# Optimization experiments

Measured on AMD Instinct MI355X. Metric: run time of the kernel, lower is better.

The kernel has to match this reference:

```python
import jax, jax.numpy as jnp
import numpy as np

MV = 16          # multivector dimension (PGA G(3,0,1))
BLADE_LEN = 9    # number of equivariant basis maps
# inner-product mask: coordinates not containing e0 (scalar, e1,e2,e3, e12,e13,e23, e123)
IP_IDX = np.array([0, 2, 3, 4, 8, 9, 10, 14])


def equi_linear(w, blade, x):
    """EquiLinearLayer: einsum('j i b, b x y, ... i x -> ... j y').
    Precompute blade-contracted weight once (fusion the kernel would do)."""
    wb = jnp.einsum('jib,bxy->jixy', w, blade)          # [J, I, MV, MV]
    return jnp.einsum('jixy,...ix->...jy', wb, x)        # [..., J, MV]


def setup_inputs() -> dict:
    key = jax.random.key(0)
    ks = jax.random.split(key, 6)
    B, N, C = 2, 2048, 64       # batch, items, mv_channels
    D, H = 64, 8                # hidden_dim, n_heads
    x = jax.random.normal(ks[0], (B, N, C, MV), dtype=jnp.float32)
    blade = jax.random.normal(ks[1], (BLADE_LEN, MV, MV), dtype=jnp.float32)
    w_q = jax.random.uniform(ks[2], (D * H, C, BLADE_LEN), dtype=jnp.float32)
    w_k = jax.random.uniform(ks[3], (D, C, BLADE_LEN), dtype=jnp.float32)
    w_v = jax.random.uniform(ks[4], (D, C, BLADE_LEN), dtype=jnp.float32)
    w_o = jax.random.uniform(ks[5], (C, D * H, BLADE_LEN), dtype=jnp.float32)
    return {"x": x, "blade": blade, "w_q": w_q, "w_k": w_k, "w_v": w_v, "w_o": w_o}


def reference(x, blade, w_q, w_k, w_v, w_o):
    B, N, C, _ = x.shape
    D = w_k.shape[0]
    H = w_q.shape[0] // D

    q = equi_linear(w_q, blade, x)   # [B, N, D*H, MV]
    k = equi_linear(w_k, blade, x)   # [B, N, D, MV]
    v = equi_linear(w_v, blade, x)   # [B, N, D, MV]

    # '(hidden_dim n_heads)' split: hidden_dim outer, heads inner
    q = q.reshape(B, N, D, H, MV).transpose(0, 3, 1, 2, 4)   # [B, H, N, D, MV]

    # select inner-product coordinates and flatten channel x coord
    qm = q[..., IP_IDX].reshape(B, H, N, D * len(IP_IDX))    # [B, H, N, D*8]
    km = k[..., IP_IDX].reshape(B, N, D * len(IP_IDX))        # [B, N, D*8]
    vf = v.reshape(B, N, D * MV)                              # [B, N, D*16]

    scale = 1.0 / jnp.sqrt(jnp.asarray(qm.shape[-1], qm.dtype))
    scores = jnp.einsum('bhqe,bke->bhqk', qm, km) * scale     # [B, H, N, N]
    attn = jax.nn.softmax(scores, axis=-1)
    out = jnp.einsum('bhqk,bkf->bhqf', attn, vf)              # [B, H, N, D*16]

    # slice first hidden_dim*mv (a no-op here since v keeps all 16 coords)
    out = out[..., : D * MV].reshape(B, H, N, D, MV)
    # '(heads hidden_dim)': heads outer
    out = out.transpose(0, 2, 1, 3, 4).reshape(B, N, H * D, MV)

    return equi_linear(w_o, blade, out)                       # [B, N, out_channels, MV]
```

## Files before the change

kernel.cpp:

```cpp
#include <hip/hip_runtime.h>
#include <math.h>


typedef __bf16 bf16x8 __attribute__((ext_vector_type(8)));
typedef __bf16 bf16x4 __attribute__((ext_vector_type(4)));
typedef float floatx4 __attribute__((ext_vector_type(4)));
typedef float floatx16 __attribute__((ext_vector_type(16)));

__constant__ int c_ip[8] = {0, 2, 3, 4, 8, 9, 10, 14};

__global__ __launch_bounds__(256) void prep2(
    const float* __restrict__ x, const float* __restrict__ blade,
    const float* __restrict__ w_q, const float* __restrict__ w_k,
    const float* __restrict__ w_v, const float* __restrict__ w_o,
    __bf16* __restrict__ xh, __bf16* __restrict__ xl,
    __bf16* __restrict__ wbqkh, __bf16* __restrict__ wbqkl,
    __bf16* __restrict__ wbv, __bf16* __restrict__ wbo)
{
  __shared__ float sw[4608];
  __shared__ float sbl[144];
  const int blk = blockIdx.x;
  const int tid = threadIdx.x;

  if (blk < 4608) {
    int n = blk;
    const float* wrow;
    int y;
    if (n < 4096) {
      int e = n & 7, d = (n >> 3) & 63, h = n >> 9;
      wrow = w_q + (size_t)(d * 8 + h) * 576;
      y = c_ip[e];
    } else {
      int n2 = n - 4096;
      int e = n2 & 7, d = n2 >> 3;
      wrow = w_k + (size_t)d * 576;
      y = c_ip[e];
    }
    for (int t = tid; t < 576; t += 256) sw[t] = wrow[t];
    if (tid < 144) sbl[tid] = blade[(tid >> 4) * 256 + (tid & 15) * 16 + y];
    __syncthreads();
#pragma unroll
    for (int kq = 0; kq < 4; kq++) {
      int k = kq * 256 + tid;
      int i = k >> 4, xx = k & 15;
      float s = 0.f;
#pragma unroll
      for (int b = 0; b < 9; b++) s += sw[i * 9 + b] * sbl[b * 16 + xx];
      __bf16 h16 = (__bf16)s;
      wbqkh[(size_t)n * 1024 + k] = h16;
      wbqkl[(size_t)n * 1024 + k] = (__bf16)(s - (float)h16);
    }
  } else if (blk < 5632) {
    int n = blk - 4608;
    int d = n >> 4, y = n & 15;
    const float* wrow = w_v + (size_t)d * 576;
    for (int t = tid; t < 576; t += 256) sw[t] = wrow[t];
    if (tid < 144) sbl[tid] = blade[(tid >> 4) * 256 + (tid & 15) * 16 + y];
    __syncthreads();
#pragma unroll
    for (int kq = 0; kq < 4; kq++) {
      int k = kq * 256 + tid;
      int i = k >> 4, xx = k & 15;
      float s = 0.f;
#pragma unroll
      for (int b = 0; b < 9; b++) s += sw[i * 9 + b] * sbl[b * 16 + xx];
      wbv[(size_t)n * 1024 + k] = (__bf16)s;
    }
  } else if (blk < 6656) {
    int n = blk - 5632;
    int c = n >> 4, y = n & 15;
    const float* wrow = w_o + (size_t)c * 4608;
    for (int t = tid; t < 4608; t += 256) sw[t] = wrow[t];
    if (tid < 144) sbl[tid] = blade[(tid >> 4) * 256 + (tid & 15) * 16 + y];
    __syncthreads();
#pragma unroll
    for (int kq = 0; kq < 32; kq++) {
      int k = kq * 256 + tid;
      int ich = (k >> 10) * 64 + ((k >> 4) & 63);
      int mv = k & 15;
      float s = 0.f;
#pragma unroll
      for (int b = 0; b < 9; b++) s += sw[ich * 9 + b] * sbl[b * 16 + mv];
      wbo[(size_t)n * 8192 + k] = (__bf16)s;
    }
  } else {
    int idx = (blk - 6656) * 256 + tid;
    float4 v = ((const float4*)x)[idx];
    bf16x4 h, l;
    h.x = (__bf16)v.x; l.x = (__bf16)(v.x - (float)h.x);
    h.y = (__bf16)v.y; l.y = (__bf16)(v.y - (float)h.y);
    h.z = (__bf16)v.z; l.z = (__bf16)(v.z - (float)h.z);
    h.w = (__bf16)v.w; l.w = (__bf16)(v.w - (float)h.w);
    *(bf16x4*)(xh + (size_t)idx * 4) = h;
    *(bf16x4*)(xl + (size_t)idx * 4) = l;
  }
}

__global__ __launch_bounds__(256) void reduce4(
    const float* __restrict__ p, float* __restrict__ out, int n)
{
  int i = (blockIdx.x * 256 + threadIdx.x) * 4;
  if (i >= n) return;
  float4 a = *(const float4*)(p + i);
  float4 b = *(const float4*)(p + (size_t)n + i);
  float4 c = *(const float4*)(p + 2 * (size_t)n + i);
  float4 d = *(const float4*)(p + 3 * (size_t)n + i);
  *(float4*)(out + i) = make_float4(a.x + b.x + c.x + d.x, a.y + b.y + c.y + d.y,
                                    a.z + b.z + c.z + d.z, a.w + b.w + c.w + d.w);
}

static __device__ __forceinline__ void gll16(const __bf16* g, __bf16* l) {
  __builtin_amdgcn_global_load_lds(
      (const __attribute__((address_space(1))) void*)g,
      (__attribute__((address_space(3))) void*)l, 16, 0, 0);
}

template <int GROUP, int TS>
static __device__ __forceinline__ void swizzle_mn(int& m0, int& n0) {
  int gn = gridDim.x;
  int flat = blockIdx.y * gn + blockIdx.x;
  int panel = flat / (GROUP * gn);
  int r = flat - panel * GROUP * gn;
  m0 = (panel * GROUP + (r % GROUP)) * TS;
  n0 = (r / GROUP) * TS;
}

static __device__ __forceinline__ int frag_off32(int row, int t, int kh) {
  return row * 32 + 8 * ((2 * t + kh) ^ ((row >> 1) & 3));
}

template <int EPI>
__global__ __launch_bounds__(256) void gemm_bf16(
    const __bf16* __restrict__ A, int lda, long long sAz,
    const __bf16* __restrict__ Bt, int ldb, long long sBz,
    void* __restrict__ C0v, int ldc, long long sCz,
    int K, float alpha)
{
  __shared__ __bf16 As[128 * 32];
  __shared__ __bf16 Bs[128 * 32];
  const int tid = threadIdx.x;
  const int wave = tid >> 6, lane = tid & 63;
  int m0, n0;
  swizzle_mn<4, 128>(m0, n0);
  A  += (size_t)blockIdx.z * sAz;
  Bt += (size_t)blockIdx.z * sBz;

  const int srow = lane >> 2;
  const int skk = 8 * ((lane & 3) ^ ((lane >> 3) & 3));
  const __bf16* gA0 = A  + (size_t)(m0 + wave * 32      + srow) * lda + skk;
  const __bf16* gA1 = A  + (size_t)(m0 + wave * 32 + 16 + srow) * lda + skk;
  const __bf16* gB0 = Bt + (size_t)(n0 + wave * 32      + srow) * ldb + skk;
  const __bf16* gB1 = Bt + (size_t)(n0 + wave * 32 + 16 + srow) * ldb + skk;
  const int ldsoff = wave * 1024;

  const int l31 = lane & 31, kh = lane >> 5;
  const int wm = (wave & 1) * 64, wn = (wave >> 1) * 64;
  int aoff[2][2], boff[2][2];
#pragma unroll
  for (int i = 0; i < 2; i++)
#pragma unroll
    for (int t = 0; t < 2; t++) {
      aoff[i][t] = frag_off32(wm + i * 32 + l31, t, kh);
      boff[i][t] = frag_off32(wn + i * 32 + l31, t, kh);
    }

  floatx16 acc[2][2];
#pragma unroll
  for (int i = 0; i < 2; i++)
#pragma unroll
    for (int j = 0; j < 2; j++)
#pragma unroll
      for (int e = 0; e < 16; e++) acc[i][j][e] = 0.f;

  for (int k0 = 0; k0 < K; k0 += 32) {
    gll16(gA0, As + ldsoff); gll16(gA1, As + ldsoff + 512);
    gll16(gB0, Bs + ldsoff); gll16(gB1, Bs + ldsoff + 512);
    gA0 += 32; gA1 += 32; gB0 += 32; gB1 += 32;
    __syncthreads();
    bf16x8 af[2][2], bfv[2][2];
#pragma unroll
    for (int i = 0; i < 2; i++)
#pragma unroll
      for (int t = 0; t < 2; t++) {
        af[i][t]  = *(const bf16x8*)(As + aoff[i][t]);
        bfv[i][t] = *(const bf16x8*)(Bs + boff[i][t]);
      }
#pragma unroll
    for (int t = 0; t < 2; t++)
#pragma unroll
      for (int i = 0; i < 2; i++)
#pragma unroll
        for (int j = 0; j < 2; j++)
          acc[i][j] = __builtin_amdgcn_mfma_f32_32x32x16_bf16(
              af[i][t], bfv[j][t], acc[i][j], 0, 0, 0);
    __syncthreads();
  }

  const int rb = m0 + wm + 4 * kh;
  const int cb = n0 + wn + l31;
#pragma unroll
  for (int i = 0; i < 2; i++) {
#pragma unroll
    for (int j = 0; j < 2; j++) {
      int c = cb + j * 32;
#pragma unroll
      for (int q = 0; q < 4; q++) {
        int r = rb + i * 32 + 8 * q;
        float v0 = acc[i][j][q * 4 + 0] * alpha;
        float v1 = acc[i][j][q * 4 + 1] * alpha;
        float v2 = acc[i][j][q * 4 + 2] * alpha;
        float v3 = acc[i][j][q * 4 + 3] * alpha;
        if (EPI == 0) {
          float* C = (float*)C0v + (size_t)blockIdx.z * sCz;
          float* p = C + (size_t)r * ldc + c;
          p[0] = v0; p[ldc] = v1; p[2 * ldc] = v2; p[3 * ldc] = v3;
        } else {
          __bf16* C = (__bf16*)C0v + (size_t)blockIdx.z * sCz;
          C[(size_t)r * ldc + c] = (__bf16)v0;
          C[(size_t)(r + 1) * ldc + c] = (__bf16)v1;
          C[(size_t)(r + 2) * ldc + c] = (__bf16)v2;
          C[(size_t)(r + 3) * ldc + c] = (__bf16)v3;
        }
      }
    }
  }
}

template <int EPI>
__global__ __launch_bounds__(256) void gemm_split(
    const __bf16* __restrict__ Ah, const __bf16* __restrict__ Al, int lda, long long sAz,
    const __bf16* __restrict__ Bh, const __bf16* __restrict__ Bl, int ldb, long long sBz,
    void* __restrict__ C0v, void* __restrict__ C1v, int ldc, long long sCz,
    int K, float alpha)
{
  __shared__ __bf16 Ash[128 * 32];
  __shared__ __bf16 Asl[128 * 32];
  __shared__ __bf16 Bsh[128 * 32];
  __shared__ __bf16 Bsl[128 * 32];
  const int tid = threadIdx.x;
  const int wave = tid >> 6, lane = tid & 63;
  int m0, n0;
  swizzle_mn<8, 128>(m0, n0);
  Ah += (size_t)blockIdx.z * sAz;
  Al += (size_t)blockIdx.z * sAz;
  Bh += (size_t)blockIdx.z * sBz;
  Bl += (size_t)blockIdx.z * sBz;

  const int srow = lane >> 2;
  const int skk = 8 * ((lane & 3) ^ ((lane >> 3) & 3));
  const size_t ao0 = (size_t)(m0 + wave * 32      + srow) * lda + skk;
  const size_t ao1 = (size_t)(m0 + wave * 32 + 16 + srow) * lda + skk;
  const size_t bo0 = (size_t)(n0 + wave * 32      + srow) * ldb + skk;
  const size_t bo1 = (size_t)(n0 + wave * 32 + 16 + srow) * ldb + skk;
  const __bf16 *gAh0 = Ah + ao0, *gAh1 = Ah + ao1;
  const __bf16 *gAl0 = Al + ao0, *gAl1 = Al + ao1;
  const __bf16 *gBh0 = Bh + bo0, *gBh1 = Bh + bo1;
  const __bf16 *gBl0 = Bl + bo0, *gBl1 = Bl + bo1;
  const int ldsoff = wave * 1024;

  const int fr = lane & 15, fq = lane >> 4;
  const int wm = (wave & 1) * 64, wn = (wave >> 1) * 64;
  int aoff[4], boff[4];
#pragma unroll
  for (int t = 0; t < 4; t++) {
    int rA = wm + t * 16 + fr;
    aoff[t] = rA * 32 + 8 * (fq ^ ((rA >> 1) & 3));
    int rB = wn + t * 16 + fr;
    boff[t] = rB * 32 + 8 * (fq ^ ((rB >> 1) & 3));
  }

  floatx4 acc[4][4];
#pragma unroll
  for (int i = 0; i < 4; i++)
#pragma unroll
    for (int j = 0; j < 4; j++) acc[i][j] = (floatx4){0.f, 0.f, 0.f, 0.f};

  for (int k0 = 0; k0 < K; k0 += 32) {
    gll16(gAh0, Ash + ldsoff); gll16(gAh1, Ash + ldsoff + 512);
    gll16(gAl0, Asl + ldsoff); gll16(gAl1, Asl + ldsoff + 512);
    gll16(gBh0, Bsh + ldsoff); gll16(gBh1, Bsh + ldsoff + 512);
    gll16(gBl0, Bsl + ldsoff); gll16(gBl1, Bsl + ldsoff + 512);
    gAh0 += 32; gAh1 += 32; gAl0 += 32; gAl1 += 32;
    gBh0 += 32; gBh1 += 32; gBl0 += 32; gBl1 += 32;
    __syncthreads();
    bf16x8 afh[4], afl[4], bfh[4], bfl[4];
#pragma unroll
    for (int t = 0; t < 4; t++) {
      afh[t] = *(const bf16x8*)(Ash + aoff[t]);
      afl[t] = *(const bf16x8*)(Asl + aoff[t]);
      bfh[t] = *(const bf16x8*)(Bsh + boff[t]);
      bfl[t] = *(const bf16x8*)(Bsl + boff[t]);
    }
#pragma unroll
    for (int i = 0; i < 4; i++)
#pragma unroll
      for (int j = 0; j < 4; j++) {
        acc[i][j] = __builtin_amdgcn_mfma_f32_16x16x32_bf16(
            afh[i], bfh[j], acc[i][j], 0, 0, 0);
        acc[i][j] = __builtin_amdgcn_mfma_f32_16x16x32_bf16(
            afl[i], bfh[j], acc[i][j], 0, 0, 0);
        acc[i][j] = __builtin_amdgcn_mfma_f32_16x16x32_bf16(
            afh[i], bfl[j], acc[i][j], 0, 0, 0);
      }
    __syncthreads();
  }

  const int rb = m0 + wm + fq * 4;
  const int cb = n0 + wn + fr;
#pragma unroll
  for (int i = 0; i < 4; i++) {
#pragma unroll
    for (int j = 0; j < 4; j++) {
      float vv[4] = {acc[i][j].x * alpha, acc[i][j].y * alpha,
                     acc[i][j].z * alpha, acc[i][j].w * alpha};
      int r = rb + i * 16, c = cb + j * 16;
      if (EPI == 0) {
        float* C = (float*)C0v + (size_t)blockIdx.z * sCz;
        float* p = C + (size_t)r * ldc + c;
        p[0] = vv[0]; p[ldc] = vv[1]; p[2 * ldc] = vv[2]; p[3 * ldc] = vv[3];
      } else {
        __bf16* Hp = (__bf16*)C0v + (size_t)blockIdx.z * sCz;
        __bf16* Lp = (__bf16*)C1v + (size_t)blockIdx.z * sCz;
#pragma unroll
        for (int t = 0; t < 4; t++) {
          size_t o = (size_t)(r + t) * ldc + c;
          __bf16 hh = (__bf16)vv[t];
          Hp[o] = hh;
          Lp[o] = (__bf16)(vv[t] - (float)hh);
        }
      }
    }
  }
}

#define MFMA1(a, b, c) c = __builtin_amdgcn_mfma_f32_16x16x32_bf16(a, b, c, 0, 0, 0)

#define MFMA_PAIR(i0, i1)                                                   \
  __builtin_amdgcn_s_setprio(1);                                            \
  _Pragma("unroll") for (int j = 0; j < 4; j++) {                           \
    MFMA1(a0h, bh[j], acc[i0][j]); MFMA1(a1h, bh[j], acc[i1][j]);           \
    MFMA1(a0l, bh[j], acc[i0][j]); MFMA1(a1l, bh[j], acc[i1][j]);           \
    MFMA1(a0h, bl[j], acc[i0][j]); MFMA1(a1h, bl[j], acc[i1][j]);           \
  }                                                                         \
  __builtin_amdgcn_s_setprio(0)

#define TILE8P(SAh, SAl, SBh, SBl, DAh, DAl, DBh, DBl, PF)                  \
  do {                                                                      \
    bf16x8 bh[4], bl[4];                                                    \
    _Pragma("unroll") for (int j = 0; j < 4; j++) {                         \
      bh[j] = *(const bf16x8*)(SBh + boff[j]);                              \
      bl[j] = *(const bf16x8*)(SBl + boff[j]);                              \
    }                                                                       \
                           \
    bf16x8 a0h = *(const bf16x8*)(SAh + aoff[0]);                           \
    bf16x8 a0l = *(const bf16x8*)(SAl + aoff[0]);                           \
    bf16x8 a1h = *(const bf16x8*)(SAh + aoff[1]);                           \
    bf16x8 a1l = *(const bf16x8*)(SAl + aoff[1]);                           \
    if (PF) { gll16(pAh0, DAh + lw); gll16(pAh1, DAh + lw + 512);           \
              pAh0 += 32; pAh1 += 32; }                                     \
    MFMA_PAIR(0, 1);                                                        \
    __builtin_amdgcn_s_barrier();                                           \
                           \
    a0h = *(const bf16x8*)(SAh + aoff[2]);                                  \
    a0l = *(const bf16x8*)(SAl + aoff[2]);                                  \
    a1h = *(const bf16x8*)(SAh + aoff[3]);                                  \
    a1l = *(const bf16x8*)(SAl + aoff[3]);                                  \
    if (PF) { gll16(pAl0, DAl + lw); gll16(pAl1, DAl + lw + 512);           \
              pAl0 += 32; pAl1 += 32; }                                     \
    MFMA_PAIR(2, 3);                                                        \
    __builtin_amdgcn_s_barrier();                                           \
                           \
    a0h = *(const bf16x8*)(SAh + aoff[4]);                                  \
    a0l = *(const bf16x8*)(SAl + aoff[4]);                                  \
    a1h = *(const bf16x8*)(SAh + aoff[5]);                                  \
    a1l = *(const bf16x8*)(SAl + aoff[5]);                                  \
    if (PF) { gll16(pBh0, DBh + lw); gll16(pBh1, DBh + lw + 512);           \
              pBh0 += 32; pBh1 += 32; }                                     \
    MFMA_PAIR(4, 5);                                                        \
    __builtin_amdgcn_s_barrier();                                           \
          \
    a0h = *(const bf16x8*)(SAh + aoff[6]);                                  \
    a0l = *(const bf16x8*)(SAl + aoff[6]);                                  \
    a1h = *(const bf16x8*)(SAh + aoff[7]);                                  \
    a1l = *(const bf16x8*)(SAl + aoff[7]);                                  \
    if (PF) { gll16(pBl0, DBl + lw); gll16(pBl1, DBl + lw + 512);           \
              pBl0 += 32; pBl1 += 32; }                                     \
    MFMA_PAIR(6, 7);                                                        \
    __syncthreads();                                                        \
  } while (0)

template <int EPI>
__global__ __launch_bounds__(512) void gemm_split_8p(
    const __bf16* __restrict__ Ah, const __bf16* __restrict__ Al, int lda, long long sAz,
    const __bf16* __restrict__ Bh, const __bf16* __restrict__ Bl, int ldb, long long sBz,
    void* __restrict__ C0v, void* __restrict__ C1v, int ldc, long long sCz,
    int K, float alpha)
{
  __shared__ __bf16 sAh0[256 * 32], sAl0[256 * 32], sBh0[256 * 32], sBl0[256 * 32];
  __shared__ __bf16 sAh1[256 * 32], sAl1[256 * 32], sBh1[256 * 32], sBl1[256 * 32];
  const int tid = threadIdx.x;
  const int wave = tid >> 6, lane = tid & 63;
  int m0, n0;
  swizzle_mn<4, 256>(m0, n0);
  Ah += (size_t)blockIdx.z * sAz;
  Al += (size_t)blockIdx.z * sAz;
  Bh += (size_t)blockIdx.z * sBz;
  Bl += (size_t)blockIdx.z * sBz;

  const int srow = lane >> 2;
  const int skk = 8 * ((lane & 3) ^ ((lane >> 3) & 3));
  const __bf16* pAh0 = Ah + (size_t)(m0 + wave * 32 + srow) * lda + skk;
  const __bf16* pAh1 = pAh0 + (size_t)16 * lda;
  const __bf16* pAl0 = Al + (size_t)(m0 + wave * 32 + srow) * lda + skk;
  const __bf16* pAl1 = pAl0 + (size_t)16 * lda;
  const __bf16* pBh0 = Bh + (size_t)(n0 + wave * 32 + srow) * ldb + skk;
  const __bf16* pBh1 = pBh0 + (size_t)16 * ldb;
  const __bf16* pBl0 = Bl + (size_t)(n0 + wave * 32 + srow) * ldb + skk;
  const __bf16* pBl1 = pBl0 + (size_t)16 * ldb;
  const int lw = wave * 1024;

  const int fr = lane & 15, fq = lane >> 4;
  const int wm = (wave >> 2) * 128, wn = (wave & 3) * 64;
  int aoff[8], boff[4];
#pragma unroll
  for (int i = 0; i < 8; i++) {
    int rA = wm + i * 16 + fr;
    aoff[i] = rA * 32 + 8 * (fq ^ ((rA >> 1) & 3));
  }
#pragma unroll
  for (int j = 0; j < 4; j++) {
    int rB = wn + j * 16 + fr;
    boff[j] = rB * 32 + 8 * (fq ^ ((rB >> 1) & 3));
  }

  floatx4 acc[8][4];
#pragma unroll
  for (int i = 0; i < 8; i++)
#pragma unroll
    for (int j = 0; j < 4; j++) acc[i][j] = (floatx4){0.f, 0.f, 0.f, 0.f};

  const int ktiles = K >> 5;

  gll16(pAh0, sAh0 + lw); gll16(pAh1, sAh0 + lw + 512); pAh0 += 32; pAh1 += 32;
  gll16(pAl0, sAl0 + lw); gll16(pAl1, sAl0 + lw + 512); pAl0 += 32; pAl1 += 32;
  gll16(pBh0, sBh0 + lw); gll16(pBh1, sBh0 + lw + 512); pBh0 += 32; pBh1 += 32;
  gll16(pBl0, sBl0 + lw); gll16(pBl1, sBl0 + lw + 512); pBl0 += 32; pBl1 += 32;
  __syncthreads();

  for (int it = 0; it < (ktiles >> 1); ++it) {
    TILE8P(sAh0, sAl0, sBh0, sBl0, sAh1, sAl1, sBh1, sBl1,
           (2 * it + 1 < ktiles));
    TILE8P(sAh1, sAl1, sBh1, sBl1, sAh0, sAl0, sBh0, sBl0,
           (2 * it + 2 < ktiles));
  }

  const int rb = m0 + wm + fq * 4;
  const int cb = n0 + wn + fr;
#pragma unroll
  for (int i = 0; i < 8; i++) {
#pragma unroll
    for (int j = 0; j < 4; j++) {
      int r = rb + i * 16, c = cb + j * 16;
      float vv[4] = {acc[i][j].x * alpha, acc[i][j].y * alpha,
                     acc[i][j].z * alpha, acc[i][j].w * alpha};
      if (EPI == 0) {
        float* C = (float*)C0v + (size_t)blockIdx.z * sCz;
        float* p = C + (size_t)r * ldc + c;
        p[0] = vv[0]; p[ldc] = vv[1]; p[2 * ldc] = vv[2]; p[3 * ldc] = vv[3];
      } else {
        __bf16* Hp = (__bf16*)C0v + (size_t)blockIdx.z * sCz;
        __bf16* Lp = (__bf16*)C1v + (size_t)blockIdx.z * sCz;
#pragma unroll
        for (int t = 0; t < 4; t++) {
          size_t o = (size_t)(r + t) * ldc + c;
          __bf16 hh = (__bf16)vv[t];
          Hp[o] = hh;
          Lp[o] = (__bf16)(vv[t] - (float)hh);
        }
      }
    }
  }
}

__global__ __launch_bounds__(256) void softmax_wave(float* __restrict__ Pf)
{
  const int wave = threadIdx.x >> 6, lane = threadIdx.x & 63;
  const size_t row = (size_t)blockIdx.x * 4 + wave;
  float* p = Pf + row * 2048;
  __bf16* q = (__bf16*)p;

  float4 v[8];
  float m = -1e30f;
#pragma unroll
  for (int t = 0; t < 8; t++) {
    v[t] = ((const float4*)p)[lane + t * 64];
    m = fmaxf(m, fmaxf(fmaxf(v[t].x, v[t].y), fmaxf(v[t].z, v[t].w)));
  }
#pragma unroll
  for (int off = 32; off; off >>= 1) m = fmaxf(m, __shfl_xor(m, off, 64));

  float s = 0.f;
#pragma unroll
  for (int t = 0; t < 8; t++) {
    v[t].x = expf(v[t].x - m); v[t].y = expf(v[t].y - m);
    v[t].z = expf(v[t].z - m); v[t].w = expf(v[t].w - m);
    s += (v[t].x + v[t].y) + (v[t].z + v[t].w);
  }
#pragma unroll
  for (int off = 32; off; off >>= 1) s += __shfl_xor(s, off, 64);
  float inv = 1.0f / s;

#pragma unroll
  for (int t = 0; t < 8; t++) {
    bf16x4 o;
    o.x = (__bf16)(v[t].x * inv); o.y = (__bf16)(v[t].y * inv);
    o.z = (__bf16)(v[t].z * inv); o.w = (__bf16)(v[t].w * inv);
    *(bf16x4*)(q + (lane + t * 64) * 4) = o;
  }
}

extern "C" void kernel_launch(void* const* d_in, const int* in_sizes, int n_in,
                              void* d_out, int out_size, void* d_ws, size_t ws_size,
                              hipStream_t stream)
{
  (void)in_sizes; (void)n_in; (void)out_size; (void)ws_size;
  const float* x     = (const float*)d_in[0];
  const float* blade = (const float*)d_in[1];
  const float* w_q   = (const float*)d_in[2];
  const float* w_k   = (const float*)d_in[3];
  const float* w_v   = (const float*)d_in[4];
  const float* w_o   = (const float*)d_in[5];
  float* out = (float*)d_out;

  char* base = (char*)d_ws;
  __bf16* wbo   = (__bf16*)(base);
  __bf16* vT    = (__bf16*)(base + 16777216);
  __bf16* qkmh  = (__bf16*)(base + 25165824);
  __bf16* qkml  = (__bf16*)(base + 62914560);
  char* scr = base + 100663296;
  __bf16* xh    = (__bf16*)(scr);
  __bf16* xl    = (__bf16*)(scr + 8388608);
  __bf16* wbqkh = (__bf16*)(scr + 16777216);
  __bf16* wbqkl = (__bf16*)(scr + 26214400);
  __bf16* wbv   = (__bf16*)(scr + 35651584);
  float*  Pf    = (float*)(scr);
  __bf16* A2    = (__bf16*)(scr + 67108864);
  float*  Part  = (float*)(scr + 100663296);

  dim3 blk(256);
  const float scale = 0.04419417382415922f;

  prep2<<<10752, blk, 0, stream>>>(x, blade, w_q, w_k, w_v, w_o,
                                   xh, xl, wbqkh, wbqkl, wbv, wbo);

  gemm_split_8p<2><<<dim3(16, 16, 1), dim3(512), 0, stream>>>(
      xh, xl, 1024, 0, wbqkh, wbqkl, 1024, 0,
      qkmh, qkml, 4608, 0, 1024, 1.f);

  gemm_split<2><<<dim3(4, 32, 1), blk, 0, stream>>>(
      xh, xl, 1024, 0,
      wbqkh + (size_t)4096 * 1024, wbqkl + (size_t)4096 * 1024, 1024, 0,
      qkmh + 4096, qkml + 4096, 4608, 0, 1024, 1.f);

  gemm_bf16<3><<<dim3(32, 8, 1), blk, 0, stream>>>(
      wbv, 1024, 0, xh, 1024, 0, vT, 4096, 0, 1024, 1.f);

  for (int b = 0; b < 2; b++) {
    const __bf16* qh_b  = qkmh + (size_t)b * 2048 * 4608;
    const __bf16* ql_b  = qkml + (size_t)b * 2048 * 4608;
    const __bf16* kmh_b = qh_b + 4096;
    const __bf16* kml_b = ql_b + 4096;

    for (int h0 = 0; h0 < 8; h0 += 4) {
      gemm_split_8p<0><<<dim3(8, 8, 4), dim3(512), 0, stream>>>(
          qh_b + h0 * 512, ql_b + h0 * 512, 4608, 512,
          kmh_b, kml_b, 4608, 0,
          Pf, nullptr, 2048, (long long)2048 * 2048, 512, scale);
      softmax_wave<<<4 * 2048 / 4, blk, 0, stream>>>(Pf);
      gemm_bf16<3><<<dim3(8, 16, 4), blk, 0, stream>>>(
          (const __bf16*)Pf, 4096, (long long)2048 * 4096,
          vT + (size_t)b * 2048, 4096, 0,
          A2 + (size_t)h0 * 1024, 8192, 1024, 2048, 1.f);
    }

    gemm_bf16<0><<<dim3(8, 16, 4), blk, 0, stream>>>(
        A2, 8192, 2048, wbo, 8192, 2048,
        Part, 1024, (long long)2048 * 1024, 2048, 1.f);
    reduce4<<<2048, blk, 0, stream>>>(Part, out + (size_t)b * 2048 * 1024,
                                      2048 * 1024);
  }
}
```

Measured before the change: 789.5 us.

## Use 8-wave double-buffered 256x128 GEMM kernel for PV and output projection

Adds a 512-thread, 8-wave bf16 MFMA GEMM with 256x128 block tiles. It double-buffers LDS using direct global-to-LDS loads interleaved with the MFMA phases, and raises wave priority around the MFMA bursts. The attention PV product and the output projection now use this kernel in place of the 256-thread gemm_bf16, so global-load latency can overlap compute and data is reused more per tile. The grid is halved, which means fewer blocks in flight, and the larger LDS footprint may cap occupancy.

New measurement: 811.5 us. 1.03x slower.

```diff
diff --git a/kernel.cpp b/kernel.cpp
--- a/kernel.cpp
+++ b/kernel.cpp
@@ -482,6 +482,125 @@
   }
 }
 
+#define PTILE(SA0, SA1, SB0, SB1, DA0, DA1, DB0, DB1, PF)                   \
+  do {                                                                      \
+    bf16x8 b0[4], b1[4];                                                    \
+    _Pragma("unroll") for (int j = 0; j < 4; j++) {                         \
+      b0[j] = *(const bf16x8*)(SB0 + boff[j]);                              \
+      b1[j] = *(const bf16x8*)(SB1 + boff[j]);                              \
+    }                                                                       \
+       \
+    bf16x8 a00 = *(const bf16x8*)(SA0 + aoff[0]);                           \
+    bf16x8 a01 = *(const bf16x8*)(SA1 + aoff[0]);                           \
+    bf16x8 a10 = *(const bf16x8*)(SA0 + aoff[1]);                           \
+    bf16x8 a11 = *(const bf16x8*)(SA1 + aoff[1]);                           \
+    if (PF) { gll16(pA0, DA0 + lw); gll16(pA1, DA0 + lw + 512);             \
+              gll16(pA0 + 32, DA1 + lw); }                                  \
+    __builtin_amdgcn_s_setprio(1);                                          \
+    _Pragma("unroll") for (int j = 0; j < 4; j++) {                         \
+      MFMA1(a00, b0[j], acc[0][j]); MFMA1(a10, b0[j], acc[1][j]);           \
+      MFMA1(a01, b1[j], acc[0][j]); MFMA1(a11, b1[j], acc[1][j]);           \
+    }                                                                       \
+    __builtin_amdgcn_s_setprio(0);                                          \
+    __builtin_amdgcn_s_barrier();                                           \
+       \
+    a00 = *(const bf16x8*)(SA0 + aoff[2]);                                  \
+    a01 = *(const bf16x8*)(SA1 + aoff[2]);                                  \
+    a10 = *(const bf16x8*)(SA0 + aoff[3]);                                  \
+    a11 = *(const bf16x8*)(SA1 + aoff[3]);                                  \
+    if (PF) { gll16(pA1 + 32, DA1 + lw + 512);                              \
+              gll16(pB0, DB0 + lwB); gll16(pB0 + 32, DB1 + lwB);            \
+              pA0 += 64; pA1 += 64; pB0 += 64; }                            \
+    __builtin_amdgcn_s_setprio(1);                                          \
+    _Pragma("unroll") for (int j = 0; j < 4; j++) {                         \
+      MFMA1(a00, b0[j], acc[2][j]); MFMA1(a10, b0[j], acc[3][j]);           \
+      MFMA1(a01, b1[j], acc[2][j]); MFMA1(a11, b1[j], acc[3][j]);           \
+    }                                                                       \
+    __builtin_amdgcn_s_setprio(0);                                          \
+    __syncthreads();                                                        \
+  } while (0)
+
+template <int EPI>
+__global__ __launch_bounds__(512) void gemm_bf16_8p(
+    const __bf16* __restrict__ A, int lda, long long sAz,
+    const __bf16* __restrict__ Bt, int ldb, long long sBz,
+    void* __restrict__ C0v, int ldc, long long sCz,
+    int K, float alpha)
+{
+  __shared__ __bf16 sA0_0[256 * 32], sA1_0[256 * 32];
+  __shared__ __bf16 sB0_0[128 * 32], sB1_0[128 * 32];
+  __shared__ __bf16 sA0_1[256 * 32], sA1_1[256 * 32];
+  __shared__ __bf16 sB0_1[128 * 32], sB1_1[128 * 32];
+  const int tid = threadIdx.x;
+  const int wave = tid >> 6, lane = tid & 63;
+  const int m0 = blockIdx.y * 256, n0 = blockIdx.x * 128;
+  A  += (size_t)blockIdx.z * sAz;
+  Bt += (size_t)blockIdx.z * sBz;
+
+  const int srow = lane >> 2;
+  const int skk = 8 * ((lane & 3) ^ ((lane >> 3) & 3));
+  const __bf16* pA0 = A + (size_t)(m0 + wave * 32 + srow) * lda + skk;
+  const __bf16* pA1 = pA0 + (size_t)16 * lda;
+  const __bf16* pB0 = Bt + (size_t)(n0 + wave * 16 + srow) * ldb + skk;
+  const int lw = wave * 1024;
+  const int lwB = wave * 512;
+
+  const int fr = lane & 15, fq = lane >> 4;
+  const int wm = (wave >> 1) * 64, wn = (wave & 1) * 64;
+  int aoff[4], boff[4];
+#pragma unroll
+  for (int i = 0; i < 4; i++) {
+    int rA = wm + i * 16 + fr;
+    aoff[i] = rA * 32 + 8 * (fq ^ ((rA >> 1) & 3));
+    int rB = wn + i * 16 + fr;
+    boff[i] = rB * 32 + 8 * (fq ^ ((rB >> 1) & 3));
+  }
+
+  floatx4 acc[4][4];
+#pragma unroll
+  for (int i = 0; i < 4; i++)
+#pragma unroll
+    for (int j = 0; j < 4; j++) acc[i][j] = (floatx4){0.f, 0.f, 0.f, 0.f};
+
+  const int ktiles = K >> 6;
+
+  gll16(pA0, sA0_0 + lw); gll16(pA1, sA0_0 + lw + 512);
+  gll16(pA0 + 32, sA1_0 + lw); gll16(pA1 + 32, sA1_0 + lw + 512);
+  gll16(pB0, sB0_0 + lwB); gll16(pB0 + 32, sB1_0 + lwB);
+  pA0 += 64; pA1 += 64; pB0 += 64;
+  __syncthreads();
+
+  for (int it = 0; it < (ktiles >> 1); ++it) {
+    PTILE(sA0_0, sA1_0, sB0_0, sB1_0, sA0_1, sA1_1, sB0_1, sB1_1,
+          (2 * it + 1 < ktiles));
+    PTILE(sA0_1, sA1_1, sB0_1, sB1_1, sA0_0, sA1_0, sB0_0, sB1_0,
+          (2 * it + 2 < ktiles));
+  }
+
+  const int rb = m0 + wm + fq * 4;
+  const int cb = n0 + wn + fr;
+#pragma unroll
+  for (int i = 0; i < 4; i++) {
+#pragma unroll
+    for (int j = 0; j < 4; j++) {
+      int r = rb + i * 16, c = cb + j * 16;
+      float vv[4] = {acc[i][j].x * alpha, acc[i][j].y * alpha,
+                     acc[i][j].z * alpha, acc[i][j].w * alpha};
+      if (EPI == 0) {
+        float* C = (float*)C0v + (size_t)blockIdx.z * sCz;
+        float* p = C + (size_t)r * ldc + c;
+        p[0] = vv[0]; p[ldc] = vv[1]; p[2 * ldc] = vv[2]; p[3 * ldc] = vv[3];
+      } else {
+        __bf16* C = (__bf16*)C0v + (size_t)blockIdx.z * sCz;
+        C[(size_t)r * ldc + c] = (__bf16)vv[0];
+        C[(size_t)(r + 1) * ldc + c] = (__bf16)vv[1];
+        C[(size_t)(r + 2) * ldc + c] = (__bf16)vv[2];
+        C[(size_t)(r + 3) * ldc + c] = (__bf16)vv[3];
+      }
+    }
+  }
+}
+
 __global__ __launch_bounds__(256) void softmax_wave(float* __restrict__ Pf)
 {
   const int wave = threadIdx.x >> 6, lane = threadIdx.x & 63;
@@ -577,13 +696,13 @@
           kmh_b, kml_b, 4608, 0,
           Pf, nullptr, 2048, (long long)2048 * 2048, 512, scale);
       softmax_wave<<<4 * 2048 / 4, blk, 0, stream>>>(Pf);
-      gemm_bf16<3><<<dim3(8, 16, 4), blk, 0, stream>>>(
+      gemm_bf16_8p<3><<<dim3(8, 8, 4), dim3(512), 0, stream>>>(
           (const __bf16*)Pf, 4096, (long long)2048 * 4096,
           vT + (size_t)b * 2048, 4096, 0,
           A2 + (size_t)h0 * 1024, 8192, 1024, 2048, 1.f);
     }
 
-    gemm_bf16<0><<<dim3(8, 16, 4), blk, 0, stream>>>(
+    gemm_bf16_8p<0><<<dim3(8, 8, 4), dim3(512), 0, stream>>>(
         A2, 8192, 2048, wbo, 8192, 2048,
         Part, 1024, (long long)2048 * 1024, 2048, 1.f);
     reduce4<<<2048, blk, 0, stream>>>(Part, out + (size_t)b * 2048 * 1024,
```

## Split-K the key projection GEMM and rebalance prefetch barriers in 8-phase tile

Applied to the files above, without the earlier changes.

The key projection GEMM now runs as a two-way split-K into float partials, followed by a new kernel that sums the partials and writes the hi/lo bf16 split into the packed q/k buffer. This is meant to fill more CUs than the small 4x32 grid did. The 8-phase tile loop also drops three intermediate s_barriers and moves the global-to-LDS prefetches earlier into the first three phases, trying to reduce synchronisation stalls. The cost is an extra kernel launch and a round trip of partials through memory, and removing the barriers risks LDS hazards. An unused swizzle helper is added as well.

Result: no change. 784.6 us (-0.6%).

```diff
diff --git a/kernel.cpp b/kernel.cpp
--- a/kernel.cpp
+++ b/kernel.cpp
@@ -109,6 +109,27 @@
                                     a.z + b.z + c.z + d.z, a.w + b.w + c.w + d.w);
 }
 
+__global__ __launch_bounds__(256) void split2km(
+    const float* __restrict__ p, __bf16* __restrict__ Hp,
+    __bf16* __restrict__ Lp)
+{
+  const int n = 4096 * 512;
+  int i = (blockIdx.x * 256 + threadIdx.x) * 4;
+  if (i >= n) return;
+  float4 a = *(const float4*)(p + i);
+  float4 b = *(const float4*)(p + (size_t)n + i);
+  float s0 = a.x + b.x, s1 = a.y + b.y, s2 = a.z + b.z, s3 = a.w + b.w;
+  int row = i >> 9, col = i & 511;
+  size_t o = (size_t)row * 4608 + col;
+  bf16x4 h, l;
+  h.x = (__bf16)s0; l.x = (__bf16)(s0 - (float)h.x);
+  h.y = (__bf16)s1; l.y = (__bf16)(s1 - (float)h.y);
+  h.z = (__bf16)s2; l.z = (__bf16)(s2 - (float)h.z);
+  h.w = (__bf16)s3; l.w = (__bf16)(s3 - (float)h.w);
+  *(bf16x4*)(Hp + o) = h;
+  *(bf16x4*)(Lp + o) = l;
+}
+
 static __device__ __forceinline__ void gll16(const __bf16* g, __bf16* l) {
   __builtin_amdgcn_global_load_lds(
       (const __attribute__((address_space(1))) void*)g,
@@ -123,6 +144,16 @@
   int r = flat - panel * GROUP * gn;
   m0 = (panel * GROUP + (r % GROUP)) * TS;
   n0 = (r / GROUP) * TS;
+}
+
+template <int GROUP, int TSM, int TSN>
+static __device__ __forceinline__ void swizzle_mn2(int& m0, int& n0) {
+  int gn = gridDim.x;
+  int flat = blockIdx.y * gn + blockIdx.x;
+  int panel = flat / (GROUP * gn);
+  int r = flat - panel * GROUP * gn;
+  m0 = (panel * GROUP + (r % GROUP)) * TSM;
+  n0 = (r / GROUP) * TSN;
 }
 
 static __device__ __forceinline__ int frag_off32(int row, int t, int kh) {
@@ -351,40 +382,37 @@
       bh[j] = *(const bf16x8*)(SBh + boff[j]);                              \
       bl[j] = *(const bf16x8*)(SBl + boff[j]);                              \
     }                                                                       \
-                           \
+            \
     bf16x8 a0h = *(const bf16x8*)(SAh + aoff[0]);                           \
     bf16x8 a0l = *(const bf16x8*)(SAl + aoff[0]);                           \
     bf16x8 a1h = *(const bf16x8*)(SAh + aoff[1]);                           \
     bf16x8 a1l = *(const bf16x8*)(SAl + aoff[1]);                           \
     if (PF) { gll16(pAh0, DAh + lw); gll16(pAh1, DAh + lw + 512);           \
-              pAh0 += 32; pAh1 += 32; }                                     \
+              gll16(pAl0, DAl + lw);                                        \
+              pAh0 += 32; pAh1 += 32; pAl0 += 32; }                         \
     MFMA_PAIR(0, 1);                                                        \
-    __builtin_amdgcn_s_barrier();                                           \
-                           \
+           \
     a0h = *(const bf16x8*)(SAh + aoff[2]);                                  \
     a0l = *(const bf16x8*)(SAl + aoff[2]);                                  \
     a1h = *(const bf16x8*)(SAh + aoff[3]);                                  \
     a1l = *(const bf16x8*)(SAl + aoff[3]);                                  \
-    if (PF) { gll16(pAl0, DAl + lw); gll16(pAl1, DAl + lw + 512);           \
-              pAl0 += 32; pAl1 += 32; }                                     \
+    if (PF) { gll16(pAl1, DAl + lw + 512);                                  \
+              gll16(pBh0, DBh + lw); gll16(pBh1, DBh + lw + 512);           \
+              pAl1 += 32; pBh0 += 32; pBh1 += 32; }                         \
     MFMA_PAIR(2, 3);                                                        \
-    __builtin_amdgcn_s_barrier();                                           \
-                           \
+                       \
     a0h = *(const bf16x8*)(SAh + aoff[4]);                                  \
     a0l = *(const bf16x8*)(SAl + aoff[4]);                                  \
     a1h = *(const bf16x8*)(SAh + aoff[5]);                                  \
     a1l = *(const bf16x8*)(SAl + aoff[5]);                                  \
-    if (PF) { gll16(pBh0, DBh + lw); gll16(pBh1, DBh + lw + 512);           \
-              pBh0 += 32; pBh1 += 32; }                                     \
+    if (PF) { gll16(pBl0, DBl + lw); gll16(pBl1, DBl + lw + 512);           \
+              pBl0 += 32; pBl1 += 32; }                                     \
     MFMA_PAIR(4, 5);                                                        \
-    __builtin_amdgcn_s_barrier();                                           \
-          \
+                  \
     a0h = *(const bf16x8*)(SAh + aoff[6]);                                  \
     a0l = *(const bf16x8*)(SAl + aoff[6]);                                  \
     a1h = *(const bf16x8*)(SAh + aoff[7]);                                  \
     a1l = *(const bf16x8*)(SAl + aoff[7]);                                  \
-    if (PF) { gll16(pBl0, DBl + lw); gll16(pBl1, DBl + lw + 512);           \
-              pBl0 += 32; pBl1 += 32; }                                     \
     MFMA_PAIR(6, 7);                                                        \
     __syncthreads();                                                        \
   } while (0)
@@ -543,6 +571,7 @@
   __bf16* wbqkh = (__bf16*)(scr + 16777216);
   __bf16* wbqkl = (__bf16*)(scr + 26214400);
   __bf16* wbv   = (__bf16*)(scr + 35651584);
+  float*  kmP   = (float*)(scr + 37748736);
   float*  Pf    = (float*)(scr);
   __bf16* A2    = (__bf16*)(scr + 67108864);
   float*  Part  = (float*)(scr + 100663296);
@@ -557,10 +586,11 @@
       xh, xl, 1024, 0, wbqkh, wbqkl, 1024, 0,
       qkmh, qkml, 4608, 0, 1024, 1.f);
 
-  gemm_split<2><<<dim3(4, 32, 1), blk, 0, stream>>>(
-      xh, xl, 1024, 0,
-      wbqkh + (size_t)4096 * 1024, wbqkl + (size_t)4096 * 1024, 1024, 0,
-      qkmh + 4096, qkml + 4096, 4608, 0, 1024, 1.f);
+  gemm_split<0><<<dim3(4, 32, 2), blk, 0, stream>>>(
+      xh, xl, 1024, 512,
+      wbqkh + (size_t)4096 * 1024, wbqkl + (size_t)4096 * 1024, 1024, 512,
+      kmP, nullptr, 512, (long long)4096 * 512, 512, 1.f);
+  split2km<<<2048, blk, 0, stream>>>(kmP, qkmh + 4096, qkml + 4096);
 
   gemm_bf16<3><<<dim3(32, 8, 1), blk, 0, stream>>>(
       wbv, 1024, 0, xh, 1024, 0, vT, 4096, 0, 1024, 1.f);
```
